# Kernel tuning notes

Measured on AMD Instinct MI355X. Metric: run time of the kernel, lower is better.

The kernel has to match this reference:

```python
import jax, jax.numpy as jnp
import numpy as np

HIDDEN = 2048
INTER = 768
NUM_EXPERTS = 32
TOP_K = 4
NUM_TOKENS = 2048


def setup_inputs() -> dict:
    key = jax.random.key(0)
    ks = jax.random.split(key, 5)
    scale = 0.02
    x = jax.random.normal(ks[0], (NUM_TOKENS, HIDDEN), dtype=jnp.float32)
    w_router = jax.random.normal(ks[1], (HIDDEN, NUM_EXPERTS), dtype=jnp.float32) * scale
    w_gate = jax.random.normal(ks[2], (NUM_EXPERTS, HIDDEN, INTER), dtype=jnp.float32) * scale
    w_up = jax.random.normal(ks[3], (NUM_EXPERTS, HIDDEN, INTER), dtype=jnp.float32) * scale
    w_down = jax.random.normal(ks[4], (NUM_EXPERTS, INTER, HIDDEN), dtype=jnp.float32) * scale
    return {"hidden_states": x, "w_router": w_router, "w_gate": w_gate,
            "w_up": w_up, "w_down": w_down}


def reference(hidden_states, w_router, w_gate, w_up, w_down):
    x = hidden_states  # [T, H]
    T = x.shape[0]
    # Router: softmax over experts (in input dtype), top-k, renormalize.
    router_logits = x @ w_router                      # [T, E]
    routing_weights = jax.nn.softmax(router_logits, axis=-1)
    top_w, top_idx = jax.lax.top_k(routing_weights, TOP_K)  # [T, K]
    top_w = top_w / jnp.sum(top_w, axis=-1, keepdims=True)   # norm_topk_prob
    # Dense combine weights: combine[t, e] = routing weight if expert e selected
    # for token t, else 0.  (top-k indices are unique per token.)
    combine = jnp.zeros((T, NUM_EXPERTS), dtype=x.dtype)
    combine = combine.at[jnp.arange(T)[:, None], top_idx].add(top_w)  # [T, E]

    # Scan over experts: each step computes one expert's SwiGLU MLP on all
    # tokens and accumulates it weighted by its combine weight (tokens with
    # zero weight contribute nothing, matching the gather/scatter original).
    def body(acc, expert):
        wg, wu, wd, cw = expert  # [H,I], [H,I], [I,H], [T]
        h = jax.nn.silu(x @ wg) * (x @ wu)   # [T, I]
        return acc + (h @ wd) * cw[:, None], None

    out, _ = jax.lax.scan(body, jnp.zeros_like(x),
                          (w_gate, w_up, w_down, combine.T))
    return out
```

## Files before the change

kernel.cpp:

```cpp
#include <hip/hip_runtime.h>

#define T_TOK 2048
#define HID   2048
#define INTER 768
#define NE    32
#define NSLOT 8192
#define MAXT  96

typedef short bf16x8 __attribute__((ext_vector_type(8)));
typedef float f32x4  __attribute__((ext_vector_type(4)));

#if defined(__has_builtin)
#  if __has_builtin(__builtin_amdgcn_global_load_lds)
#    define HAS_GLDS 1
#  endif
#endif
#ifndef HAS_GLDS
#  define HAS_GLDS 0
#endif

__device__ __forceinline__ unsigned short f2b(float f){
  unsigned u = __builtin_bit_cast(unsigned, f);
  u += 0x7fffu + ((u >> 16) & 1u);
  return (unsigned short)(u >> 16);
}
__device__ __forceinline__ unsigned pk2(float a, float b){
  return (unsigned)f2b(a) | ((unsigned)f2b(b) << 16);
}
__device__ __forceinline__ float b2f(unsigned short u){
  unsigned x = ((unsigned)u) << 16;
  return __builtin_bit_cast(float, x);
}

__device__ __forceinline__ void stageA16(const ushort* gsrc, ushort* ldst){
#if HAS_GLDS
  __builtin_amdgcn_global_load_lds(
      (const __attribute__((address_space(1))) unsigned int*)gsrc,
      (__attribute__((address_space(3))) unsigned int*)ldst, 16, 0, 0);
#else
  *(uint4*)ldst = *(const uint4*)gsrc;
#endif
}

#define XB_OFF    0ul
#define GBUF_OFF  8388608ul
#define TKW_OFF   20971520ul
#define TKI_OFF   21004288ul
#define ROWS_OFF  21037056ul
#define WTS_OFF   21069824ul
#define OFFS_OFF  21102592ul
#define LOGIT_OFF 21102848ul
#define CNT_OFF   21364992ul
#define FILL_OFF  21365120ul
#define TLIST_OFF 21365248ul
#define UBUF_OFF  21365760ul
#define ZERO_OFF  21102848ul
#define ZERO_SZ   (262144ul + 128ul + 128ul)

__global__ void convert_x_kernel(const float* __restrict__ x, ushort* __restrict__ xb){
  int i = (blockIdx.x * 256 + threadIdx.x) * 8;
  float4 a = *(const float4*)(x + i);
  float4 b = *(const float4*)(x + i + 4);
  uint4 o;
  o.x = pk2(a.x, a.y);
  o.y = pk2(a.z, a.w);
  o.z = pk2(b.x, b.y);
  o.w = pk2(b.z, b.w);
  *(uint4*)(xb + i) = o;
}

__global__ void router_gemm(const float* __restrict__ x, const float* __restrict__ wr,
                            float* __restrict__ logits){
  const int tt = blockIdx.x;
  const int kb = blockIdx.y;
  __shared__ float xs[64 * 64];
  __shared__ float wsm[64 * 32];
  const int tid = threadIdx.x;
  const int r = tid >> 5, e = tid & 31;
  float acc[8];
#pragma unroll
  for (int i = 0; i < 8; i++) acc[i] = 0.0f;

  for (int sub = 0; sub < 4; ++sub){
    const int k0 = kb * 256 + sub * 64;
    __syncthreads();
#pragma unroll
    for (int j = 0; j < 4; j++){
      int f4 = tid + j * 256;
      int row = f4 >> 4, c4 = f4 & 15;
      float4 v = *(const float4*)(x + (size_t)(tt * 64 + row) * HID + k0 + c4 * 4);
      *(float4*)(xs + row * 64 + c4 * 4) = v;
    }
#pragma unroll
    for (int j = 0; j < 2; j++){
      int f4 = tid + j * 256;
      int row = f4 >> 3, c4 = f4 & 7;
      float4 v = *(const float4*)(wr + (size_t)(k0 + row) * NE + c4 * 4);
      *(float4*)(wsm + row * NE + c4 * 4) = v;
    }
    __syncthreads();
    for (int kk = 0; kk < 64; kk++){
      float wv = wsm[kk * NE + e];
#pragma unroll
      for (int i = 0; i < 8; i++) acc[i] += xs[(r + i * 8) * 64 + kk] * wv;
    }
  }
#pragma unroll
  for (int i = 0; i < 8; i++)
    atomicAdd(&logits[(size_t)(tt * 64 + r + i * 8) * NE + e], acc[i]);
}

__global__ void topk_kernel(const float* __restrict__ logits, float* __restrict__ topk_w,
                            int* __restrict__ topk_i, int* __restrict__ counts){
  int t = blockIdx.x * blockDim.x + threadIdx.x;
  if (t >= T_TOK) return;
  float l[32];
  const float4* lp = (const float4*)(logits + (size_t)t * NE);
#pragma unroll
  for (int i = 0; i < 8; i++){
    float4 v = lp[i];
    l[i*4+0] = v.x; l[i*4+1] = v.y; l[i*4+2] = v.z; l[i*4+3] = v.w;
  }
  float m = l[0];
#pragma unroll
  for (int i = 1; i < 32; i++) m = fmaxf(m, l[i]);
#pragma unroll
  for (int i = 0; i < 32; i++) l[i] = __expf(l[i] - m);
  float wsel[4]; int isel[4];
#pragma unroll
  for (int k = 0; k < 4; k++){
    float best = l[0]; int bi = 0;
#pragma unroll
    for (int i = 1; i < 32; i++){ if (l[i] > best){ best = l[i]; bi = i; } }
    wsel[k] = best; isel[k] = bi; l[bi] = -1.0f;
  }
  float s4 = wsel[0] + wsel[1] + wsel[2] + wsel[3];
  float inv = 1.0f / s4;
#pragma unroll
  for (int k = 0; k < 4; k++){
    topk_w[t * 4 + k] = wsel[k] * inv;
    topk_i[t * 4 + k] = isel[k];
    atomicAdd(&counts[isel[k]], 1);
  }
}

__global__ void prefix_kernel(const int* __restrict__ counts, int* __restrict__ offsets,
                              int* __restrict__ tlist){
  if (threadIdx.x == 0){
    int a = 0; offsets[0] = 0; int nt_ = 0;
    for (int e = 0; e < NE; e++){
      int c = counts[e];
      for (int m = 0; m * 128 < c && nt_ < MAXT; m++) tlist[nt_++] = e | (m << 16);
      a += c; offsets[e + 1] = a;
    }
    for (; nt_ < MAXT; nt_++) tlist[nt_] = -1;
  }
}

__global__ void scatter_kernel(const int* __restrict__ topk_i, const float* __restrict__ topk_w,
                               const int* __restrict__ offsets, int* __restrict__ fill,
                               int* __restrict__ rows, float* __restrict__ wts){
  int gid = blockIdx.x * 256 + threadIdx.x;
  int t = gid >> 2;
  int e = topk_i[gid];
  int pos = atomicAdd(&fill[e], 1);
  int s = offsets[e] + pos;
  rows[s] = t;
  wts[s] = topk_w[gid];
}

#define NT_GU 64
#define LDS_STRIDE 12288
__global__ __launch_bounds__(512) void guv_kernel(
    const ushort* __restrict__ xb, const float* __restrict__ wg,
    const float* __restrict__ wu, const int* __restrict__ rows,
    const int* __restrict__ counts, const int* __restrict__ offsets,
    const int* __restrict__ tlist, ushort* __restrict__ gbuf,
    ushort* __restrict__ ubuf)
{
  const int w = tlist[blockIdx.y];
  if (w < 0) return;
  const int e = w & 0xffff, mt = w >> 16;
  const int mat = blockIdx.x & 1, nt = blockIdx.x >> 1;
  const int cnt = counts[e], off = offsets[e];
  const int n0 = nt * 256;

  __shared__ __align__(16) ushort lds[2 * LDS_STRIDE + 4096];

  const int tid = threadIdx.x;
  const int lane = tid & 63, wv = tid >> 6;

  const int ar = tid >> 2;
  const int aq = (tid & 3) ^ (ar & 3);
  const int srow = mt * 128 + ar;
  const int tokA = rows[off + (srow < cnt ? srow : 0)];
  const ushort* agp = xb + (size_t)tokA * HID + aq * 8;

  const float* wsel = mat ? wu : wg;
  const float* bgp = wsel + (size_t)e * (HID * INTER) + (size_t)(wv * 4) * INTER + n0 + lane * 4;
  const int bwbase = lane * 128 + ((wv ^ ((lane & 3) << 1)) << 2);

  const int wm = wv >> 2, wn = wv & 3;
  const int fr = lane & 15, ko = lane >> 4;
  int aoff[4], boff[4];
#pragma unroll
  for (int mf = 0; mf < 4; mf++){
    int r = wm * 64 + mf * 16 + fr;
    aoff[mf] = r * 32 + ((ko ^ (r & 3)) << 3);
  }
#pragma unroll
  for (int nf = 0; nf < 4; nf++){
    int c = wn * 64 + nf * 16 + fr;
    boff[nf] = c * 32 + (((ko * 2) ^ (((c >> 2) & 3) << 1)) << 2);
  }

  f32x4 acc[4][4];
#pragma unroll
  for (int i = 0; i < 4; i++)
#pragma unroll
    for (int j = 0; j < 4; j++) acc[i][j] = (f32x4)(0.0f);

  float4 br0, br1, br2, br3;

  auto loadB = [&](int k0){
    br0 = *(const float4*)(bgp + (size_t)(k0 + 0) * INTER);
    br1 = *(const float4*)(bgp + (size_t)(k0 + 1) * INTER);
    br2 = *(const float4*)(bgp + (size_t)(k0 + 2) * INTER);
    br3 = *(const float4*)(bgp + (size_t)(k0 + 3) * INTER);
  };
  auto writeB = [&](int cb){
    ushort* bd = lds + cb + 4096;
#pragma unroll
    for (int i = 0; i < 4; i++){
      uint2 p;
      p.x = pk2((&br0.x)[i], (&br1.x)[i]);
      p.y = pk2((&br2.x)[i], (&br3.x)[i]);
      *(uint2*)(bd + bwbase + i * 32) = p;
    }
  };
  auto compute = [&](int cb){
    const ushort* A = lds + cb;
    const ushort* B = lds + cb + 4096;
    bf16x8 a[4], b[4];
#pragma unroll
    for (int mf = 0; mf < 4; mf++) a[mf] = *(const bf16x8*)(A + aoff[mf]);
#pragma unroll
    for (int nf = 0; nf < 4; nf++) b[nf] = *(const bf16x8*)(B + boff[nf]);
#pragma unroll
    for (int mf = 0; mf < 4; mf++)
#pragma unroll
      for (int nf = 0; nf < 4; nf++)
        acc[mf][nf] = __builtin_amdgcn_mfma_f32_16x16x32_bf16(a[mf], b[nf], acc[mf][nf], 0, 0, 0);
  };

  stageA16(agp, lds + tid * 8);
  loadB(0);
  writeB(0);
  __syncthreads();

  int cb = 0;
  for (int t = 0; t < NT_GU; ++t){
    const int nb = cb ^ LDS_STRIDE;
    if (t + 1 < NT_GU){
      stageA16(agp + (t + 1) * 32, lds + nb + tid * 8);
      loadB((t + 1) * 32);
    }
    compute(cb);
    if (t + 1 < NT_GU) writeB(nb);
    __syncthreads();
    cb = nb;
  }

  ushort* obuf = mat ? ubuf : gbuf;
#pragma unroll
  for (int mf = 0; mf < 4; mf++)
#pragma unroll
    for (int j = 0; j < 4; j++){
      int rl = wm * 64 + mf * 16 + ko * 4 + j;
      int gr = mt * 128 + rl;
      if (gr < cnt){
        size_t rb = (size_t)(off + gr) * INTER + n0;
#pragma unroll
        for (int nf = 0; nf < 4; nf++)
          obuf[rb + wn * 64 + nf * 16 + fr] = f2b(acc[mf][nf][j]);
      }
    }
}

__global__ void fuse_kernel(ushort* __restrict__ gbuf, const ushort* __restrict__ ubuf,
                            const float* __restrict__ wts){
  const int s = blockIdx.x;
  const int c = threadIdx.x * 4;
  const float wt = wts[s];
  size_t base = (size_t)s * INTER + c;
  uint2 gv = *(const uint2*)(gbuf + base);
  uint2 uv = *(const uint2*)(ubuf + base);
  float h[4];
  {
    float g0 = b2f((unsigned short)gv.x),        u0 = b2f((unsigned short)uv.x);
    float g1 = b2f((unsigned short)(gv.x >> 16)), u1 = b2f((unsigned short)(uv.x >> 16));
    float g2 = b2f((unsigned short)gv.y),        u2 = b2f((unsigned short)uv.y);
    float g3 = b2f((unsigned short)(gv.y >> 16)), u3 = b2f((unsigned short)(uv.y >> 16));
    h[0] = (g0 / (1.0f + __expf(-g0))) * u0 * wt;
    h[1] = (g1 / (1.0f + __expf(-g1))) * u1 * wt;
    h[2] = (g2 / (1.0f + __expf(-g2))) * u2 * wt;
    h[3] = (g3 / (1.0f + __expf(-g3))) * u3 * wt;
  }
  uint2 o; o.x = pk2(h[0], h[1]); o.y = pk2(h[2], h[3]);
  *(uint2*)(gbuf + base) = o;
}

#define NT_DN 24
__global__ __launch_bounds__(512) void down_kernel(
    const ushort* __restrict__ hbuf, const float* __restrict__ wd,
    const int* __restrict__ rows, const int* __restrict__ counts,
    const int* __restrict__ offsets, const int* __restrict__ tlist,
    float* __restrict__ out)
{
  const int w = tlist[blockIdx.y];
  if (w < 0) return;
  const int e = w & 0xffff, mt = w >> 16;
  const int nt = blockIdx.x;
  const int cnt = counts[e], off = offsets[e];
  const int n0 = nt * 256;

  __shared__ __align__(16) ushort lds[2 * LDS_STRIDE + 4096];

  const int tid = threadIdx.x;
  const int lane = tid & 63, wv = tid >> 6;

  const int ar = tid >> 2;
  const int aq = (tid & 3) ^ (ar & 3);
  const int srow = mt * 128 + ar;
  const int slotA = off + (srow < cnt ? srow : 0);
  const ushort* agp = hbuf + (size_t)slotA * INTER + aq * 8;

  const float* bgp = wd + (size_t)e * (INTER * HID) + (size_t)(wv * 4) * HID + n0 + lane * 4;
  const int bwbase = lane * 128 + ((wv ^ ((lane & 3) << 1)) << 2);

  const int wm = wv >> 2, wn = wv & 3;
  const int fr = lane & 15, ko = lane >> 4;
  int aoff[4], boff[4];
#pragma unroll
  for (int mf = 0; mf < 4; mf++){
    int r = wm * 64 + mf * 16 + fr;
    aoff[mf] = r * 32 + ((ko ^ (r & 3)) << 3);
  }
#pragma unroll
  for (int nf = 0; nf < 4; nf++){
    int c = wn * 64 + nf * 16 + fr;
    boff[nf] = c * 32 + (((ko * 2) ^ (((c >> 2) & 3) << 1)) << 2);
  }

  f32x4 acc[4][4];
#pragma unroll
  for (int i = 0; i < 4; i++)
#pragma unroll
    for (int j = 0; j < 4; j++) acc[i][j] = (f32x4)(0.0f);

  float4 br0, br1, br2, br3;

  auto loadB = [&](int k0){
    br0 = *(const float4*)(bgp + (size_t)(k0 + 0) * HID);
    br1 = *(const float4*)(bgp + (size_t)(k0 + 1) * HID);
    br2 = *(const float4*)(bgp + (size_t)(k0 + 2) * HID);
    br3 = *(const float4*)(bgp + (size_t)(k0 + 3) * HID);
  };
  auto writeB = [&](int cb){
    ushort* bd = lds + cb + 4096;
#pragma unroll
    for (int i = 0; i < 4; i++){
      uint2 p;
      p.x = pk2((&br0.x)[i], (&br1.x)[i]);
      p.y = pk2((&br2.x)[i], (&br3.x)[i]);
      *(uint2*)(bd + bwbase + i * 32) = p;
    }
  };
  auto compute = [&](int cb){
    const ushort* A = lds + cb;
    const ushort* B = lds + cb + 4096;
    bf16x8 a[4], b[4];
#pragma unroll
    for (int mf = 0; mf < 4; mf++) a[mf] = *(const bf16x8*)(A + aoff[mf]);
#pragma unroll
    for (int nf = 0; nf < 4; nf++) b[nf] = *(const bf16x8*)(B + boff[nf]);
#pragma unroll
    for (int mf = 0; mf < 4; mf++)
#pragma unroll
      for (int nf = 0; nf < 4; nf++)
        acc[mf][nf] = __builtin_amdgcn_mfma_f32_16x16x32_bf16(a[mf], b[nf], acc[mf][nf], 0, 0, 0);
  };

  stageA16(agp, lds + tid * 8);
  loadB(0);
  writeB(0);
  __syncthreads();

  int cb = 0;
  for (int t = 0; t < NT_DN; ++t){
    const int nb = cb ^ LDS_STRIDE;
    if (t + 1 < NT_DN){
      stageA16(agp + (t + 1) * 32, lds + nb + tid * 8);
      loadB((t + 1) * 32);
    }
    compute(cb);
    if (t + 1 < NT_DN) writeB(nb);
    __syncthreads();
    cb = nb;
  }

#pragma unroll
  for (int mf = 0; mf < 4; mf++)
#pragma unroll
    for (int j = 0; j < 4; j++){
      int rl = wm * 64 + mf * 16 + ko * 4 + j;
      int gr = mt * 128 + rl;
      if (gr < cnt){
        int tok = rows[off + gr];
        float* obase = out + (size_t)tok * HID + n0;
#pragma unroll
        for (int nf = 0; nf < 4; nf++)
          atomicAdd(obase + wn * 64 + nf * 16 + fr, acc[mf][nf][j]);
      }
    }
}

extern "C" void kernel_launch(void* const* d_in, const int* in_sizes, int n_in,
                              void* d_out, int out_size, void* d_ws, size_t ws_size,
                              hipStream_t stream){
  const float* x  = (const float*)d_in[0];
  const float* wr = (const float*)d_in[1];
  const float* wg = (const float*)d_in[2];
  const float* wu = (const float*)d_in[3];
  const float* wd = (const float*)d_in[4];
  float* out = (float*)d_out;
  char* ws = (char*)d_ws;

  ushort* xb     = (ushort*)(ws + XB_OFF);
  ushort* gbuf   = (ushort*)(ws + GBUF_OFF);
  ushort* ubuf   = (ushort*)(ws + UBUF_OFF);
  float*  topkw  = (float*)(ws + TKW_OFF);
  int*    topki  = (int*)(ws + TKI_OFF);
  int*    rows   = (int*)(ws + ROWS_OFF);
  float*  wts    = (float*)(ws + WTS_OFF);
  int*    offs   = (int*)(ws + OFFS_OFF);
  float*  logits = (float*)(ws + LOGIT_OFF);
  int*    counts = (int*)(ws + CNT_OFF);
  int*    fill   = (int*)(ws + FILL_OFF);
  int*    tlist  = (int*)(ws + TLIST_OFF);

  hipMemsetAsync(ws + ZERO_OFF, 0, ZERO_SZ, stream);
  hipMemsetAsync(d_out, 0, (size_t)out_size * sizeof(float), stream);

  convert_x_kernel<<<2048, 256, 0, stream>>>(x, xb);
  router_gemm<<<dim3(32, 8), 256, 0, stream>>>(x, wr, logits);
  topk_kernel<<<8, 256, 0, stream>>>(logits, topkw, topki, counts);
  prefix_kernel<<<1, 64, 0, stream>>>(counts, offs, tlist);
  scatter_kernel<<<32, 256, 0, stream>>>(topki, topkw, offs, fill, rows, wts);
  guv_kernel<<<dim3(6, MAXT), 512, 0, stream>>>(xb, wg, wu, rows, counts, offs, tlist, gbuf, ubuf);
  fuse_kernel<<<NSLOT, 192, 0, stream>>>(gbuf, ubuf, wts);
  down_kernel<<<dim3(8, MAXT), 512, 0, stream>>>(gbuf, wd, rows, counts, offs, tlist, out);
}
```

Baseline: 356.3 us.

## Halve gate/up GEMM N-tile, shrink LDS, and re-swizzle B tile layout

```diff
diff --git a/kernel.cpp b/kernel.cpp
--- a/kernel.cpp
+++ b/kernel.cpp
@@ -41,6 +41,8 @@
   *(uint4*)ldst = *(const uint4*)gsrc;
 #endif
 }
+
+__device__ __forceinline__ int HB(int c){ return ((c >> 2) ^ (c >> 4)) & 3; }
 
 #define XB_OFF    0ul
 #define GBUF_OFF  8388608ul
@@ -170,7 +172,7 @@
 }
 
 #define NT_GU 64
-#define LDS_STRIDE 12288
+#define GUV_STRIDE 8192
 __global__ __launch_bounds__(512) void guv_kernel(
     const ushort* __restrict__ xb, const float* __restrict__ wg,
     const float* __restrict__ wu, const int* __restrict__ rows,
@@ -180,12 +182,14 @@
 {
   const int w = tlist[blockIdx.y];
   if (w < 0) return;
+  const int x = blockIdx.x;
+  if (x >= 12) return;
   const int e = w & 0xffff, mt = w >> 16;
-  const int mat = blockIdx.x & 1, nt = blockIdx.x >> 1;
+  const int mat = x & 1, nt = x >> 1;
   const int cnt = counts[e], off = offsets[e];
-  const int n0 = nt * 256;
-
-  __shared__ __align__(16) ushort lds[2 * LDS_STRIDE + 4096];
+  const int n0 = nt * 128;
+
+  __shared__ __align__(16) ushort lds[2 * GUV_STRIDE];
 
   const int tid = threadIdx.x;
   const int lane = tid & 63, wv = tid >> 6;
@@ -197,59 +201,60 @@
   const ushort* agp = xb + (size_t)tokA * HID + aq * 8;
 
   const float* wsel = mat ? wu : wg;
-  const float* bgp = wsel + (size_t)e * (HID * INTER) + (size_t)(wv * 4) * INTER + n0 + lane * 4;
-  const int bwbase = lane * 128 + ((wv ^ ((lane & 3) << 1)) << 2);
+  const int bl = lane & 31;
+  const int brow = 4 * wv + 2 * (lane >> 5);
+  const float* bgp = wsel + (size_t)e * (HID * INTER) + (size_t)brow * INTER + n0 + bl * 4;
+  const int Qc = wv >> 1;
+  const int wrd = (2 * wv + (lane >> 5)) & 3;
 
   const int wm = wv >> 2, wn = wv & 3;
   const int fr = lane & 15, ko = lane >> 4;
-  int aoff[4], boff[4];
+  int aoff[4], boff[2];
 #pragma unroll
   for (int mf = 0; mf < 4; mf++){
     int r = wm * 64 + mf * 16 + fr;
     aoff[mf] = r * 32 + ((ko ^ (r & 3)) << 3);
   }
 #pragma unroll
-  for (int nf = 0; nf < 4; nf++){
-    int c = wn * 64 + nf * 16 + fr;
-    boff[nf] = c * 32 + (((ko * 2) ^ (((c >> 2) & 3) << 1)) << 2);
-  }
-
-  f32x4 acc[4][4];
+  for (int nf = 0; nf < 2; nf++){
+    int c = wn * 32 + nf * 16 + fr;
+    boff[nf] = c * 32 + ((ko ^ HB(c)) << 3);
+  }
+
+  f32x4 acc[4][2];
 #pragma unroll
   for (int i = 0; i < 4; i++)
 #pragma unroll
-    for (int j = 0; j < 4; j++) acc[i][j] = (f32x4)(0.0f);
-
-  float4 br0, br1, br2, br3;
+    for (int j = 0; j < 2; j++) acc[i][j] = (f32x4)(0.0f);
+
+  float4 br0, br1;
 
   auto loadB = [&](int k0){
     br0 = *(const float4*)(bgp + (size_t)(k0 + 0) * INTER);
     br1 = *(const float4*)(bgp + (size_t)(k0 + 1) * INTER);
-    br2 = *(const float4*)(bgp + (size_t)(k0 + 2) * INTER);
-    br3 = *(const float4*)(bgp + (size_t)(k0 + 3) * INTER);
   };
   auto writeB = [&](int cb){
-    ushort* bd = lds + cb + 4096;
+    uint* bd = (uint*)(lds + cb + 4096);
 #pragma unroll
     for (int i = 0; i < 4; i++){
-      uint2 p;
-      p.x = pk2((&br0.x)[i], (&br1.x)[i]);
-      p.y = pk2((&br2.x)[i], (&br3.x)[i]);
-      *(uint2*)(bd + bwbase + i * 32) = p;
+      int ii = i ^ (lane & 3);
+      int c = bl * 4 + ii;
+      bd[c * 16 + ((Qc ^ HB(c)) << 2) + wrd] =
+          pk2(((const float*)&br0)[ii], ((const float*)&br1)[ii]);
     }
   };
   auto compute = [&](int cb){
     const ushort* A = lds + cb;
     const ushort* B = lds + cb + 4096;
-    bf16x8 a[4], b[4];
+    bf16x8 a[4], b[2];
 #pragma unroll
     for (int mf = 0; mf < 4; mf++) a[mf] = *(const bf16x8*)(A + aoff[mf]);
 #pragma unroll
-    for (int nf = 0; nf < 4; nf++) b[nf] = *(const bf16x8*)(B + boff[nf]);
+    for (int nf = 0; nf < 2; nf++) b[nf] = *(const bf16x8*)(B + boff[nf]);
 #pragma unroll
     for (int mf = 0; mf < 4; mf++)
 #pragma unroll
-      for (int nf = 0; nf < 4; nf++)
+      for (int nf = 0; nf < 2; nf++)
         acc[mf][nf] = __builtin_amdgcn_mfma_f32_16x16x32_bf16(a[mf], b[nf], acc[mf][nf], 0, 0, 0);
   };
 
@@ -260,7 +265,7 @@
 
   int cb = 0;
   for (int t = 0; t < NT_GU; ++t){
-    const int nb = cb ^ LDS_STRIDE;
+    const int nb = cb ^ GUV_STRIDE;
     if (t + 1 < NT_GU){
       stageA16(agp + (t + 1) * 32, lds + nb + tid * 8);
       loadB((t + 1) * 32);
@@ -281,8 +286,8 @@
       if (gr < cnt){
         size_t rb = (size_t)(off + gr) * INTER + n0;
 #pragma unroll
-        for (int nf = 0; nf < 4; nf++)
-          obuf[rb + wn * 64 + nf * 16 + fr] = f2b(acc[mf][nf][j]);
+        for (int nf = 0; nf < 2; nf++)
+          obuf[rb + wn * 32 + nf * 16 + fr] = f2b(acc[mf][nf][j]);
       }
     }
 }
@@ -311,6 +316,7 @@
 }
 
 #define NT_DN 24
+#define DN_STRIDE 12288
 __global__ __launch_bounds__(512) void down_kernel(
     const ushort* __restrict__ hbuf, const float* __restrict__ wd,
     const int* __restrict__ rows, const int* __restrict__ counts,
@@ -324,7 +330,7 @@
   const int cnt = counts[e], off = offsets[e];
   const int n0 = nt * 256;
 
-  __shared__ __align__(16) ushort lds[2 * LDS_STRIDE + 4096];
+  __shared__ __align__(16) ushort lds[2 * DN_STRIDE];
 
   const int tid = threadIdx.x;
   const int lane = tid & 63, wv = tid >> 6;
@@ -336,7 +342,8 @@
   const ushort* agp = hbuf + (size_t)slotA * INTER + aq * 8;
 
   const float* bgp = wd + (size_t)e * (INTER * HID) + (size_t)(wv * 4) * HID + n0 + lane * 4;
-  const int bwbase = lane * 128 + ((wv ^ ((lane & 3) << 1)) << 2);
+  const int Qc = wv >> 1;
+  const int wb2 = ((2 * wv) & 3) << 1;
 
   const int wm = wv >> 2, wn = wv & 3;
   const int fr = lane & 15, ko = lane >> 4;
@@ -349,7 +356,7 @@
 #pragma unroll
   for (int nf = 0; nf < 4; nf++){
     int c = wn * 64 + nf * 16 + fr;
-    boff[nf] = c * 32 + (((ko * 2) ^ (((c >> 2) & 3) << 1)) << 2);
+    boff[nf] = c * 32 + ((ko ^ HB(c)) << 3);
   }
 
   f32x4 acc[4][4];
@@ -370,10 +377,12 @@
     ushort* bd = lds + cb + 4096;
 #pragma unroll
     for (int i = 0; i < 4; i++){
+      int ii = i ^ (lane & 3);
+      int c = lane * 4 + ii;
       uint2 p;
-      p.x = pk2((&br0.x)[i], (&br1.x)[i]);
-      p.y = pk2((&br2.x)[i], (&br3.x)[i]);
-      *(uint2*)(bd + bwbase + i * 32) = p;
+      p.x = pk2(((const float*)&br0)[ii], ((const float*)&br1)[ii]);
+      p.y = pk2(((const float*)&br2)[ii], ((const float*)&br3)[ii]);
+      *(uint2*)(bd + c * 32 + ((Qc ^ HB(c)) << 3) + wb2) = p;
     }
   };
   auto compute = [&](int cb){
@@ -398,7 +407,7 @@
 
   int cb = 0;
   for (int t = 0; t < NT_DN; ++t){
-    const int nb = cb ^ LDS_STRIDE;
+    const int nb = cb ^ DN_STRIDE;
     if (t + 1 < NT_DN){
       stageA16(agp + (t + 1) * 32, lds + nb + tid * 8);
       loadB((t + 1) * 32);
@@ -457,7 +466,7 @@
   topk_kernel<<<8, 256, 0, stream>>>(logits, topkw, topki, counts);
   prefix_kernel<<<1, 64, 0, stream>>>(counts, offs, tlist);
   scatter_kernel<<<32, 256, 0, stream>>>(topki, topkw, offs, fill, rows, wts);
-  guv_kernel<<<dim3(6, MAXT), 512, 0, stream>>>(xb, wg, wu, rows, counts, offs, tlist, gbuf, ubuf);
+  guv_kernel<<<dim3(16, MAXT), 512, 0, stream>>>(xb, wg, wu, rows, counts, offs, tlist, gbuf, ubuf);
   fuse_kernel<<<NSLOT, 192, 0, stream>>>(gbuf, ubuf, wts);
   down_kernel<<<dim3(8, MAXT), 512, 0, stream>>>(gbuf, wd, rows, counts, offs, tlist, out);
 }
```

Result: slower. 643.3 us (+80.5%).

## Prefetch two K-tiles in registers with padded LDS layout in expert GEMMs

Applied to the files above, without the earlier changes.

```diff
diff --git a/kernel.cpp b/kernel.cpp
--- a/kernel.cpp
+++ b/kernel.cpp
@@ -10,15 +10,6 @@
 typedef short bf16x8 __attribute__((ext_vector_type(8)));
 typedef float f32x4  __attribute__((ext_vector_type(4)));
 
-#if defined(__has_builtin)
-#  if __has_builtin(__builtin_amdgcn_global_load_lds)
-#    define HAS_GLDS 1
-#  endif
-#endif
-#ifndef HAS_GLDS
-#  define HAS_GLDS 0
-#endif
-
 __device__ __forceinline__ unsigned short f2b(float f){
   unsigned u = __builtin_bit_cast(unsigned, f);
   u += 0x7fffu + ((u >> 16) & 1u);
@@ -32,14 +23,10 @@
   return __builtin_bit_cast(float, x);
 }
 
-__device__ __forceinline__ void stageA16(const ushort* gsrc, ushort* ldst){
-#if HAS_GLDS
-  __builtin_amdgcn_global_load_lds(
-      (const __attribute__((address_space(1))) unsigned int*)gsrc,
-      (__attribute__((address_space(3))) unsigned int*)ldst, 16, 0, 0);
-#else
-  *(uint4*)ldst = *(const uint4*)gsrc;
-#endif
+__device__ __forceinline__ void wgbar(){
+  asm volatile("s_waitcnt lgkmcnt(0)" ::: "memory");
+  __builtin_amdgcn_s_barrier();
+  __builtin_amdgcn_sched_barrier(0);
 }
 
 #define XB_OFF    0ul
@@ -170,8 +157,9 @@
 }
 
 #define NT_GU 64
-#define LDS_STRIDE 12288
-__global__ __launch_bounds__(512) void guv_kernel(
+#define A_USH 5120
+#define BUF_USH 15360
+__global__ __launch_bounds__(512, 2) void guv_kernel(
     const ushort* __restrict__ xb, const float* __restrict__ wg,
     const float* __restrict__ wu, const int* __restrict__ rows,
     const int* __restrict__ counts, const int* __restrict__ offsets,
@@ -185,34 +173,28 @@
   const int cnt = counts[e], off = offsets[e];
   const int n0 = nt * 256;
 
-  __shared__ __align__(16) ushort lds[2 * LDS_STRIDE + 4096];
+  __shared__ __align__(16) ushort lds[2 * BUF_USH];
 
   const int tid = threadIdx.x;
   const int lane = tid & 63, wv = tid >> 6;
 
-  const int ar = tid >> 2;
-  const int aq = (tid & 3) ^ (ar & 3);
+  const int ar = tid >> 2, ablk = tid & 3;
   const int srow = mt * 128 + ar;
   const int tokA = rows[off + (srow < cnt ? srow : 0)];
-  const ushort* agp = xb + (size_t)tokA * HID + aq * 8;
+  const ushort* agp = xb + (size_t)tokA * HID + ablk * 8;
+  const int adst = ar * 40 + ablk * 8;
 
   const float* wsel = mat ? wu : wg;
-  const float* bgp = wsel + (size_t)e * (HID * INTER) + (size_t)(wv * 4) * INTER + n0 + lane * 4;
-  const int bwbase = lane * 128 + ((wv ^ ((lane & 3) << 1)) << 2);
+  const float* bgp = wsel + (size_t)e * (HID * INTER) + (size_t)(wv * 4) * INTER + n0 + lane;
+  const int bdst = A_USH + lane * 40 + wv * 4;
 
   const int wm = wv >> 2, wn = wv & 3;
   const int fr = lane & 15, ko = lane >> 4;
   int aoff[4], boff[4];
 #pragma unroll
-  for (int mf = 0; mf < 4; mf++){
-    int r = wm * 64 + mf * 16 + fr;
-    aoff[mf] = r * 32 + ((ko ^ (r & 3)) << 3);
-  }
-#pragma unroll
-  for (int nf = 0; nf < 4; nf++){
-    int c = wn * 64 + nf * 16 + fr;
-    boff[nf] = c * 32 + (((ko * 2) ^ (((c >> 2) & 3) << 1)) << 2);
-  }
+  for (int mf = 0; mf < 4; mf++) aoff[mf] = (wm * 64 + mf * 16 + fr) * 40 + ko * 8;
+#pragma unroll
+  for (int nf = 0; nf < 4; nf++) boff[nf] = A_USH + (wn * 64 + nf * 16 + fr) * 40 + ko * 8;
 
   f32x4 acc[4][4];
 #pragma unroll
@@ -220,32 +202,31 @@
 #pragma unroll
     for (int j = 0; j < 4; j++) acc[i][j] = (f32x4)(0.0f);
 
-  float4 br0, br1, br2, br3;
-
-  auto loadB = [&](int k0){
-    br0 = *(const float4*)(bgp + (size_t)(k0 + 0) * INTER);
-    br1 = *(const float4*)(bgp + (size_t)(k0 + 1) * INTER);
-    br2 = *(const float4*)(bgp + (size_t)(k0 + 2) * INTER);
-    br3 = *(const float4*)(bgp + (size_t)(k0 + 3) * INTER);
-  };
-  auto writeB = [&](int cb){
-    ushort* bd = lds + cb + 4096;
+  uint4 a0, a1; uint2 b0[4], b1[4];
+
+  auto loadSet = [&](int k0, uint4 &aa, uint2 *bb){
+    aa = *(const uint4*)(agp + k0);
 #pragma unroll
     for (int i = 0; i < 4; i++){
-      uint2 p;
-      p.x = pk2((&br0.x)[i], (&br1.x)[i]);
-      p.y = pk2((&br2.x)[i], (&br3.x)[i]);
-      *(uint2*)(bd + bwbase + i * 32) = p;
-    }
-  };
-  auto compute = [&](int cb){
-    const ushort* A = lds + cb;
-    const ushort* B = lds + cb + 4096;
+      float v0 = bgp[(size_t)(k0 + 0) * INTER + i * 64];
+      float v1 = bgp[(size_t)(k0 + 1) * INTER + i * 64];
+      float v2 = bgp[(size_t)(k0 + 2) * INTER + i * 64];
+      float v3 = bgp[(size_t)(k0 + 3) * INTER + i * 64];
+      bb[i].x = pk2(v0, v1); bb[i].y = pk2(v2, v3);
+    }
+  };
+  auto writeSet = [&](int base, const uint4 &aa, const uint2 *bb){
+    *(uint4*)(lds + base + adst) = aa;
+#pragma unroll
+    for (int i = 0; i < 4; i++)
+      *(uint2*)(lds + base + bdst + i * 2560) = bb[i];
+  };
+  auto compute = [&](int base){
     bf16x8 a[4], b[4];
 #pragma unroll
-    for (int mf = 0; mf < 4; mf++) a[mf] = *(const bf16x8*)(A + aoff[mf]);
-#pragma unroll
-    for (int nf = 0; nf < 4; nf++) b[nf] = *(const bf16x8*)(B + boff[nf]);
+    for (int mf = 0; mf < 4; mf++) a[mf] = *(const bf16x8*)(lds + base + aoff[mf]);
+#pragma unroll
+    for (int nf = 0; nf < 4; nf++) b[nf] = *(const bf16x8*)(lds + base + boff[nf]);
 #pragma unroll
     for (int mf = 0; mf < 4; mf++)
 #pragma unroll
@@ -253,22 +234,19 @@
         acc[mf][nf] = __builtin_amdgcn_mfma_f32_16x16x32_bf16(a[mf], b[nf], acc[mf][nf], 0, 0, 0);
   };
 
-  stageA16(agp, lds + tid * 8);
-  loadB(0);
-  writeB(0);
-  __syncthreads();
-
-  int cb = 0;
-  for (int t = 0; t < NT_GU; ++t){
-    const int nb = cb ^ LDS_STRIDE;
-    if (t + 1 < NT_GU){
-      stageA16(agp + (t + 1) * 32, lds + nb + tid * 8);
-      loadB((t + 1) * 32);
-    }
-    compute(cb);
-    if (t + 1 < NT_GU) writeB(nb);
-    __syncthreads();
-    cb = nb;
+  loadSet(0, a0, b0);
+  loadSet(32, a1, b1);
+  writeSet(0, a0, b0);
+  wgbar();
+
+  for (int t = 0; t < NT_GU; t += 2){
+    if (t + 2 < NT_GU) loadSet((t + 2) * 32, a0, b0);
+    compute(0);
+    writeSet(BUF_USH, a1, b1);
+    wgbar();
+    if (t + 3 < NT_GU) loadSet((t + 3) * 32, a1, b1);
+    compute(BUF_USH);
+    if (t + 2 < NT_GU){ writeSet(0, a0, b0); wgbar(); }
   }
 
   ushort* obuf = mat ? ubuf : gbuf;
@@ -311,7 +289,7 @@
 }
 
 #define NT_DN 24
-__global__ __launch_bounds__(512) void down_kernel(
+__global__ __launch_bounds__(512, 2) void down_kernel(
     const ushort* __restrict__ hbuf, const float* __restrict__ wd,
     const int* __restrict__ rows, const int* __restrict__ counts,
     const int* __restrict__ offsets, const int* __restrict__ tlist,
@@ -324,33 +302,27 @@
   const int cnt = counts[e], off = offsets[e];
   const int n0 = nt * 256;
 
-  __shared__ __align__(16) ushort lds[2 * LDS_STRIDE + 4096];
+  __shared__ __align__(16) ushort lds[2 * BUF_USH];
 
   const int tid = threadIdx.x;
   const int lane = tid & 63, wv = tid >> 6;
 
-  const int ar = tid >> 2;
-  const int aq = (tid & 3) ^ (ar & 3);
+  const int ar = tid >> 2, ablk = tid & 3;
   const int srow = mt * 128 + ar;
   const int slotA = off + (srow < cnt ? srow : 0);
-  const ushort* agp = hbuf + (size_t)slotA * INTER + aq * 8;
-
-  const float* bgp = wd + (size_t)e * (INTER * HID) + (size_t)(wv * 4) * HID + n0 + lane * 4;
-  const int bwbase = lane * 128 + ((wv ^ ((lane & 3) << 1)) << 2);
+  const ushort* agp = hbuf + (size_t)slotA * INTER + ablk * 8;
+  const int adst = ar * 40 + ablk * 8;
+
+  const float* bgp = wd + (size_t)e * (INTER * HID) + (size_t)(wv * 4) * HID + n0 + lane;
+  const int bdst = A_USH + lane * 40 + wv * 4;
 
   const int wm = wv >> 2, wn = wv & 3;
   const int fr = lane & 15, ko = lane >> 4;
   int aoff[4], boff[4];
 #pragma unroll
-  for (int mf = 0; mf < 4; mf++){
-    int r = wm * 64 + mf * 16 + fr;
-    aoff[mf] = r * 32 + ((ko ^ (r & 3)) << 3);
-  }
-#pragma unroll
-  for (int nf = 0; nf < 4; nf++){
-    int c = wn * 64 + nf * 16 + fr;
-    boff[nf] = c * 32 + (((ko * 2) ^ (((c >> 2) & 3) << 1)) << 2);
-  }
+  for (int mf = 0; mf < 4; mf++) aoff[mf] = (wm * 64 + mf * 16 + fr) * 40 + ko * 8;
+#pragma unroll
+  for (int nf = 0; nf < 4; nf++) boff[nf] = A_USH + (wn * 64 + nf * 16 + fr) * 40 + ko * 8;
 
   f32x4 acc[4][4];
 #pragma unroll
@@ -358,32 +330,31 @@
 #pragma unroll
     for (int j = 0; j < 4; j++) acc[i][j] = (f32x4)(0.0f);
 
-  float4 br0, br1, br2, br3;
-
-  auto loadB = [&](int k0){
-    br0 = *(const float4*)(bgp + (size_t)(k0 + 0) * HID);
-    br1 = *(const float4*)(bgp + (size_t)(k0 + 1) * HID);
-    br2 = *(const float4*)(bgp + (size_t)(k0 + 2) * HID);
-    br3 = *(const float4*)(bgp + (size_t)(k0 + 3) * HID);
-  };
-  auto writeB = [&](int cb){
-    ushort* bd = lds + cb + 4096;
+  uint4 a0, a1; uint2 b0[4], b1[4];
+
+  auto loadSet = [&](int k0, uint4 &aa, uint2 *bb){
+    aa = *(const uint4*)(agp + k0);
 #pragma unroll
     for (int i = 0; i < 4; i++){
-      uint2 p;
-      p.x = pk2((&br0.x)[i], (&br1.x)[i]);
-      p.y = pk2((&br2.x)[i], (&br3.x)[i]);
-      *(uint2*)(bd + bwbase + i * 32) = p;
-    }
-  };
-  auto compute = [&](int cb){
-    const ushort* A = lds + cb;
-    const ushort* B = lds + cb + 4096;
+      float v0 = bgp[(size_t)(k0 + 0) * HID + i * 64];
+      float v1 = bgp[(size_t)(k0 + 1) * HID + i * 64];
+      float v2 = bgp[(size_t)(k0 + 2) * HID + i * 64];
+      float v3 = bgp[(size_t)(k0 + 3) * HID + i * 64];
+      bb[i].x = pk2(v0, v1); bb[i].y = pk2(v2, v3);
+    }
+  };
+  auto writeSet = [&](int base, const uint4 &aa, const uint2 *bb){
+    *(uint4*)(lds + base + adst) = aa;
+#pragma unroll
+    for (int i = 0; i < 4; i++)
+      *(uint2*)(lds + base + bdst + i * 2560) = bb[i];
+  };
+  auto compute = [&](int base){
     bf16x8 a[4], b[4];
 #pragma unroll
-    for (int mf = 0; mf < 4; mf++) a[mf] = *(const bf16x8*)(A + aoff[mf]);
-#pragma unroll
-    for (int nf = 0; nf < 4; nf++) b[nf] = *(const bf16x8*)(B + boff[nf]);
+    for (int mf = 0; mf < 4; mf++) a[mf] = *(const bf16x8*)(lds + base + aoff[mf]);
+#pragma unroll
+    for (int nf = 0; nf < 4; nf++) b[nf] = *(const bf16x8*)(lds + base + boff[nf]);
 #pragma unroll
     for (int mf = 0; mf < 4; mf++)
 #pragma unroll
@@ -391,22 +362,19 @@
         acc[mf][nf] = __builtin_amdgcn_mfma_f32_16x16x32_bf16(a[mf], b[nf], acc[mf][nf], 0, 0, 0);
   };
 
-  stageA16(agp, lds + tid * 8);
-  loadB(0);
-  writeB(0);
-  __syncthreads();
-
-  int cb = 0;
-  for (int t = 0; t < NT_DN; ++t){
-    const int nb = cb ^ LDS_STRIDE;
-    if (t + 1 < NT_DN){
-      stageA16(agp + (t + 1) * 32, lds + nb + tid * 8);
-      loadB((t + 1) * 32);
-    }
-    compute(cb);
-    if (t + 1 < NT_DN) writeB(nb);
-    __syncthreads();
-    cb = nb;
+  loadSet(0, a0, b0);
+  loadSet(32, a1, b1);
+  writeSet(0, a0, b0);
+  wgbar();
+
+  for (int t = 0; t < NT_DN; t += 2){
+    if (t + 2 < NT_DN) loadSet((t + 2) * 32, a0, b0);
+    compute(0);
+    writeSet(BUF_USH, a1, b1);
+    wgbar();
+    if (t + 3 < NT_DN) loadSet((t + 3) * 32, a1, b1);
+    compute(BUF_USH);
+    if (t + 2 < NT_DN){ writeSet(0, a0, b0); wgbar(); }
   }
 
 #pragma unroll
```

New measurement: 374.4 us. 1.05x slower.
